# Kernel tuning notes

Hardware: AMD Instinct MI355X
Metric: run time of the kernel (lower is better)

## Reference

```python
import jax, jax.numpy as jnp
import numpy as np

B, K, H = 8, 64, 2048
NH, NKV, HD = 16, 4, 128
CTX = 4096
EPS = 1e-6


def _rope_tables(batch, total_len, head_dim):
    inv_freq = 1.0 / (10000.0 ** (np.arange(0, head_dim, 2, dtype=np.float32) / head_dim))
    pos = np.arange(total_len, dtype=np.float32)
    freqs = np.outer(pos, inv_freq)                      # [S, D/2]
    emb = np.concatenate([freqs, freqs], axis=-1)        # [S, D]
    cos = np.broadcast_to(np.cos(emb), (batch, total_len, head_dim))
    sin = np.broadcast_to(np.sin(emb), (batch, total_len, head_dim))
    return jnp.asarray(cos), jnp.asarray(sin)


def setup_inputs() -> dict:
    key = jax.random.key(0)
    ks = jax.random.split(key, 10)
    s = 0.02
    cos, sin = _rope_tables(B, CTX + K, HD)
    return {
        "hidden_states": jax.random.normal(ks[0], (B, K, H), jnp.float32),
        "ctx_k": jax.random.normal(ks[1], (B, CTX, NKV, HD), jnp.float32),
        "ctx_v": jax.random.normal(ks[2], (B, CTX, NKV, HD), jnp.float32),
        "attn_mask": jnp.zeros((B, 1, K, CTX + K), jnp.float32),
        "cos": cos,
        "sin": sin,
        "wq": jax.random.normal(ks[3], (NH * HD, H), jnp.float32) * s,
        "wk": jax.random.normal(ks[4], (NKV * HD, H), jnp.float32) * s,
        "wv": jax.random.normal(ks[5], (NKV * HD, H), jnp.float32) * s,
        "wo": jax.random.normal(ks[6], (H, NH * HD), jnp.float32) * s,
        "q_norm_w": jnp.ones((HD,), jnp.float32),
        "k_norm_w": jnp.ones((HD,), jnp.float32),
    }


def _rms_norm(x, w):
    var = jnp.mean(jnp.square(x), axis=-1, keepdims=True)
    return x * jax.lax.rsqrt(var + EPS) * w


def _rotate_half(x):
    x1, x2 = jnp.split(x, 2, axis=-1)
    return jnp.concatenate([-x2, x1], axis=-1)


def reference(hidden_states, ctx_k, ctx_v, attn_mask, cos, sin,
              wq, wk, wv, wo, q_norm_w, k_norm_w):
    b, k_len, _ = hidden_states.shape
    ctx_len = ctx_k.shape[1]
    groups = NH // NKV

    # projections -> [B, heads, S, D]
    q = (hidden_states @ wq.T).reshape(b, k_len, NH, HD).transpose(0, 2, 1, 3)
    k_noise = (hidden_states @ wk.T).reshape(b, k_len, NKV, HD).transpose(0, 2, 1, 3)
    v_noise = (hidden_states @ wv.T).reshape(b, k_len, NKV, HD).transpose(0, 2, 1, 3)

    # concat context KV (already per-head projected) with noise KV
    k = jnp.concatenate([ctx_k.transpose(0, 2, 1, 3), k_noise], axis=2)  # [B,NKV,ctx+K,D]
    v = jnp.concatenate([ctx_v.transpose(0, 2, 1, 3), v_noise], axis=2)

    # QK RMSNorm over head_dim
    q = _rms_norm(q, q_norm_w)
    k = _rms_norm(k, k_norm_w)

    # RoPE: q occupies the last K positions, k spans all ctx+K positions
    cos_q = cos[:, ctx_len:, :][:, None, :, :]
    sin_q = sin[:, ctx_len:, :][:, None, :, :]
    cos_k = cos[:, None, :, :]
    sin_k = sin[:, None, :, :]
    q = q * cos_q + _rotate_half(q) * sin_q
    k = k * cos_k + _rotate_half(k) * sin_k

    # GQA expand kv heads -> NH heads
    k = jnp.repeat(k, groups, axis=1)  # [B,NH,ctx+K,D]
    v = jnp.repeat(v, groups, axis=1)

    # scaled dot product attention with float mask
    scale = 1.0 / jnp.sqrt(jnp.float32(HD))
    scores = jnp.einsum("bhqd,bhkd->bhqk", q, k) * scale + attn_mask
    probs = jax.nn.softmax(scores, axis=-1)
    attn = jnp.einsum("bhqk,bhkd->bhqd", probs, v)

    out = attn.transpose(0, 2, 1, 3).reshape(b, k_len, NH * HD)
    return out @ wo.T
```

## Files before the change

### kernel.cpp

```cpp
#include <hip/hip_runtime.h>

#define BB   8
#define KQ   64
#define HDIM 2048
#define NH   16
#define NKV  4
#define HD   128
#define CTX  4096
#define TTOT 4160
#define NTILES 65
#define LOG2E 1.4426950408889634f
#define SCALE 0.08838834764831845f
#define QSCALE (SCALE * LOG2E)
#define MFIX 16.34f

typedef unsigned short u16;
typedef unsigned int   u32;
typedef __attribute__((ext_vector_type(8))) short  s16x8;
typedef __attribute__((ext_vector_type(4))) unsigned short u16x4;
typedef __attribute__((ext_vector_type(4))) float  f32x4;
typedef __bf16 bf16x8 __attribute__((ext_vector_type(8)));

__device__ __forceinline__ u16 f2bf(float f) {
    union { __bf16 h; u16 u; } v; v.h = (__bf16)f; return v.u;
}
__device__ __forceinline__ float bf2f(u16 u) {
    union { float f; u32 u; } v; v.u = ((u32)u) << 16;
    return v.f;
}
__device__ __forceinline__ u32 pack2(float a, float b) {
    return (u32)f2bf(a) | ((u32)f2bf(b) << 16);
}
__device__ __forceinline__ f32x4 mfma16(bf16x8 a, bf16x8 b, f32x4 c) {
    return __builtin_amdgcn_mfma_f32_16x16x32_bf16(a, b, c, 0, 0, 0);
}

__global__ __launch_bounds__(256) void cast_all(
    const float* __restrict__ wq, const float* __restrict__ wk,
    const float* __restrict__ wv, const float* __restrict__ wo,
    const float* __restrict__ hs, const float* __restrict__ cosT,
    const float* __restrict__ sinT,
    u16* __restrict__ wqkvb, u16* __restrict__ wob, u16* __restrict__ hsb,
    u16* __restrict__ cosb, u16* __restrict__ sinb)
{
    const int i = blockIdx.x * 256 + threadIdx.x;
    const float* src; u16* dst;
    if (i < 524288)        { src = wq + (size_t)i * 8;             dst = wqkvb + (size_t)i * 8; }
    else if (i < 655360)   { src = wk + (size_t)(i - 524288) * 8;  dst = wqkvb + (size_t)i * 8; }
    else if (i < 786432)   { src = wv + (size_t)(i - 655360) * 8;  dst = wqkvb + (size_t)i * 8; }
    else if (i < 1310720)  { src = wo + (size_t)(i - 786432) * 8;  dst = wob + (size_t)(i - 786432) * 8; }
    else if (i < 1441792)  { src = hs + (size_t)(i - 1310720) * 8; dst = hsb + (size_t)(i - 1310720) * 8; }
    else if (i < 1475072)  { const int l = (i - 1441792) * 8;
                             src = cosT + (size_t)(l >> 6) * 128 + (l & 63); dst = cosb + l; }
    else                   { const int l = (i - 1475072) * 8;
                             src = sinT + (size_t)(l >> 6) * 128 + (l & 63); dst = sinb + l; }
    float4 a = *(const float4*)src;
    float4 b = *(const float4*)(src + 4);
    s16x8 v;
    v[0]=(short)f2bf(a.x); v[1]=(short)f2bf(a.y); v[2]=(short)f2bf(a.z); v[3]=(short)f2bf(a.w);
    v[4]=(short)f2bf(b.x); v[5]=(short)f2bf(b.y); v[6]=(short)f2bf(b.z); v[7]=(short)f2bf(b.w);
    *(s16x8*)dst = v;
}

__global__ __launch_bounds__(256) void prep_mask(
    const float* __restrict__ mask, u16* __restrict__ maskT)
{
    __shared__ float T[64 * 65];
    const int pt = blockIdx.x % 65, b = blockIdx.x / 65;
    const int p0 = pt * 64;
    {
        const int q = threadIdx.x >> 2, pg = (threadIdx.x & 3) * 16;
        const float* src = mask + ((size_t)b * 64 + q) * TTOT + p0 + pg;
#pragma unroll
        for (int v4 = 0; v4 < 4; ++v4) {
            float4 v = *(const float4*)(src + v4 * 4);
            T[q * 65 + pg + v4 * 4 + 0] = fmaf(v.x, LOG2E, -MFIX);
            T[q * 65 + pg + v4 * 4 + 1] = fmaf(v.y, LOG2E, -MFIX);
            T[q * 65 + pg + v4 * 4 + 2] = fmaf(v.z, LOG2E, -MFIX);
            T[q * 65 + pg + v4 * 4 + 3] = fmaf(v.w, LOG2E, -MFIX);
        }
    }
    __syncthreads();
    {
        const int pos = threadIdx.x >> 2, qg = (threadIdx.x & 3) * 16;
        u16* dst = maskT + ((size_t)b * TTOT + p0 + pos) * 64 + qg;
#pragma unroll
        for (int h8 = 0; h8 < 2; ++h8) {
            s16x8 v;
#pragma unroll
            for (int je = 0; je < 8; ++je)
                v[je] = (short)f2bf(T[(qg + h8 * 8 + je) * 65 + pos]);
            *(s16x8*)(dst + h8 * 8) = v;
        }
    }
}

__device__ __forceinline__ void gemm64_body(
    const u16* __restrict__ Ab, const u16* __restrict__ Bb,
    float* __restrict__ Cb, const int ldc, const int ldk, const int Klen,
    u16* Ash, u16* Bsh)
{
    const int tid = threadIdx.x, lane = tid & 63;
    const int w = tid >> 6, wm = w >> 1, wn = w & 1;
    const int l15 = lane & 15, l4 = lane >> 4;
    const int srow = tid >> 2, scol = (tid & 3) * 16;

    f32x4 acc[2][2];
#pragma unroll
    for (int i = 0; i < 2; ++i)
#pragma unroll
        for (int j = 0; j < 2; ++j) acc[i][j] = (f32x4){0.f, 0.f, 0.f, 0.f};

    const u16* ap = Ab + (size_t)srow * ldk + scol;
    const u16* bp = Bb + (size_t)srow * ldk + scol;
    s16x8 ra0 = *(const s16x8*)ap, ra1 = *(const s16x8*)(ap + 8);
    s16x8 rb0 = *(const s16x8*)bp, rb1 = *(const s16x8*)(bp + 8);
    __builtin_amdgcn_sched_barrier(0);

    for (int k0 = 0; k0 < Klen; k0 += 64) {
        __syncthreads();
        *(s16x8*)(Ash + srow * 72 + scol)     = ra0;
        *(s16x8*)(Ash + srow * 72 + scol + 8) = ra1;
        *(s16x8*)(Bsh + srow * 72 + scol)     = rb0;
        *(s16x8*)(Bsh + srow * 72 + scol + 8) = rb1;
        __syncthreads();
        if (k0 + 64 < Klen) {
            const u16* ap2 = ap + k0 + 64;
            const u16* bp2 = bp + k0 + 64;
            ra0 = *(const s16x8*)ap2; ra1 = *(const s16x8*)(ap2 + 8);
            rb0 = *(const s16x8*)bp2; rb1 = *(const s16x8*)(bp2 + 8);
            __builtin_amdgcn_sched_barrier(0);
        }
#pragma unroll
        for (int ks = 0; ks < 2; ++ks) {
            bf16x8 am[2], bb[2];
#pragma unroll
            for (int i = 0; i < 2; ++i) {
                am[i] = *(const bf16x8*)(Ash + (wm * 32 + i * 16 + l15) * 72 + ks * 32 + l4 * 8);
                bb[i] = *(const bf16x8*)(Bsh + (wn * 32 + i * 16 + l15) * 72 + ks * 32 + l4 * 8);
            }
#pragma unroll
            for (int i = 0; i < 2; ++i)
#pragma unroll
                for (int j = 0; j < 2; ++j)
                    acc[i][j] = mfma16(am[i], bb[j], acc[i][j]);
        }
    }

    float* Cw = Cb + (size_t)(wm * 32) * ldc + wn * 32;
#pragma unroll
    for (int i = 0; i < 2; ++i)
#pragma unroll
        for (int j = 0; j < 2; ++j)
#pragma unroll
            for (int r = 0; r < 4; ++r)
                Cw[(size_t)(i * 16 + l4 * 4 + r) * ldc + j * 16 + l15] = acc[i][j][r];
}

__global__ __launch_bounds__(256) void gemm_qkv_sk(
    const u16* __restrict__ hsb, const u16* __restrict__ wqkvb,
    float* __restrict__ qkvp)
{
    __shared__ __align__(16) u16 Ash[64 * 72];
    __shared__ __align__(16) u16 Bsh[64 * 72];
    const int wid = (blockIdx.x & 7) * 192 + (blockIdx.x >> 3);
    const int y = wid >> 5, rem = wid & 31, kc = rem >> 3, x = rem & 7;
    const int koff = kc * 512;
    const u16* Ab = hsb + (size_t)x * 64 * HDIM + koff;
    const u16* Bb = wqkvb + (size_t)y * 64 * HDIM + koff;
    float* Cb = qkvp + (size_t)kc * 512 * 3072 + (size_t)x * 64 * 3072 + y * 64;
    gemm64_body(Ab, Bb, Cb, 3072, HDIM, 512, Ash, Bsh);
}

__global__ __launch_bounds__(256) void gemm_out_sk(
    const u16* __restrict__ attnb, const u16* __restrict__ wob,
    float* __restrict__ outp)
{
    __shared__ __align__(16) u16 Ash[64 * 72];
    __shared__ __align__(16) u16 Bsh[64 * 72];
    const int wid = (blockIdx.x & 7) * 128 + (blockIdx.x >> 3);
    const int y = wid >> 5, rem = wid & 31, kc = rem >> 3, x = rem & 7;
    const int koff = kc * 512;
    const u16* Ab = attnb + (size_t)x * 64 * HDIM + koff;
    const u16* Bb = wob + (size_t)y * 64 * HDIM + koff;
    float* Cb = outp + (size_t)kc * 512 * 2048 + (size_t)x * 64 * 2048 + y * 64;
    gemm64_body(Ab, Bb, Cb, 2048, HDIM, 512, Ash, Bsh);
}

__global__ __launch_bounds__(256) void reduce4(
    const float* __restrict__ p, float* __restrict__ out, const size_t chunk)
{
    const size_t i = ((size_t)blockIdx.x * 256 + threadIdx.x) * 4;
    float4 a = *(const float4*)(p + i);
    float4 b = *(const float4*)(p + i + chunk);
    float4 c = *(const float4*)(p + i + 2 * chunk);
    float4 d = *(const float4*)(p + i + 3 * chunk);
    float4 r;
    r.x = (a.x + b.x) + (c.x + d.x);
    r.y = (a.y + b.y) + (c.y + d.y);
    r.z = (a.z + b.z) + (c.z + d.z);
    r.w = (a.w + b.w) + (c.w + d.w);
    *(float4*)(out + i) = r;
}

__device__ __forceinline__ void norm_rope_vals(
    float2 xa, float2 xb, const float* __restrict__ wgt,
    const float* __restrict__ cosT, const float* __restrict__ sinT,
    int pos, int j, float outScale, u16* __restrict__ dst)
{
    float ss = xa.x * xa.x + xa.y * xa.y + xb.x * xb.x + xb.y * xb.y;
#pragma unroll
    for (int m = 1; m < 32; m <<= 1) ss += __shfl_xor(ss, m);
    const float rr = rsqrtf(ss * (1.0f / 128.0f) + 1e-6f);
    float2 wa = *(const float2*)(wgt + 2 * j);
    float2 wb = *(const float2*)(wgt + 2 * j + 64);
    float2 ca = *(const float2*)(cosT + (size_t)pos * 128 + 2 * j);
    float2 sa = *(const float2*)(sinT + (size_t)pos * 128 + 2 * j);
    const float nax = xa.x * rr * wa.x, nay = xa.y * rr * wa.y;
    const float nbx = xb.x * rr * wb.x, nby = xb.y * rr * wb.y;
    const float lox = (nax * ca.x - nbx * sa.x) * outScale;
    const float loy = (nay * ca.y - nby * sa.y) * outScale;
    const float hix = (nbx * ca.x + nax * sa.x) * outScale;
    const float hiy = (nby * ca.y + nay * sa.y) * outScale;
    ((u32*)dst)[j]      = pack2(lox, loy);
    ((u32*)dst)[j + 32] = pack2(hix, hiy);
}

__global__ __launch_bounds__(256) void finalize_qkv(
    const float* __restrict__ qkvp, const float* __restrict__ qw,
    const float* __restrict__ kw, const float* __restrict__ cosT,
    const float* __restrict__ sinT,
    u16* __restrict__ Qb, u16* __restrict__ knb, u16* __restrict__ vnb)
{
    const int unit = blockIdx.x * 8 + (threadIdx.x >> 5);
    const int j = threadIdx.x & 31;
    const int slot = unit % 24, bq = unit / 24;
    const int b = bq >> 6, q = bq & 63;
    const int col0 = (slot < 16) ? slot * 128
                   : (slot < 20) ? 2048 + (slot - 16) * 128
                                 : 2560 + (slot - 20) * 128;
    const float* base = qkvp + (size_t)bq * 3072 + col0;

    float2 xa = {0.f, 0.f}, xb = {0.f, 0.f};
#pragma unroll
    for (int kc = 0; kc < 4; ++kc) {
        const float* p = base + (size_t)kc * 512 * 3072;
        float2 a = *(const float2*)(p + 2 * j);
        float2 c = *(const float2*)(p + 2 * j + 64);
        xa.x += a.x; xa.y += a.y; xb.x += c.x; xb.y += c.y;
    }

    if (slot < 16) {
        norm_rope_vals(xa, xb, qw, cosT, sinT, CTX + q, j, QSCALE,
                       Qb + ((size_t)((b * 16 + slot) * 64 + q)) * 128);
    } else if (slot < 20) {
        norm_rope_vals(xa, xb, kw, cosT, sinT, CTX + q, j, 1.0f,
                       knb + ((size_t)((b * 4 + (slot - 16)) * 64 + q)) * 128);
    } else {
        u16* dst = vnb + ((size_t)((b * 4 + (slot - 20)) * 64 + q)) * 128;
        ((u32*)dst)[j]      = pack2(xa.x, xa.y);
        ((u32*)dst)[j + 32] = pack2(xb.x, xb.y);
    }
}

__global__ __launch_bounds__(256) void build_ctx_v(
    const float* __restrict__ ctxv, const u16* __restrict__ vnb,
    u16* __restrict__ VtG)
{
    __shared__ __align__(16) float Vt[64 * 130];
    const int bid = blockIdx.x;
    if (bid < 2048) {
        const int pt = bid & 63, kv = (bid >> 6) & 3, b = bid >> 8;
        const int p0 = pt * 64;
        const float* src = ctxv + ((size_t)(b * 4096 + p0) * 4 + kv) * 128;
#pragma unroll
        for (int it = 0; it < 8; ++it) {
            const int g = it * 256 + threadIdx.x;
            const int row = g >> 5, c4 = (g & 31) * 4;
            *(float4*)(&Vt[row * 130 + c4]) = *(const float4*)(src + (size_t)row * 512 + c4);
        }
        __syncthreads();
        const int d = threadIdx.x & 127, half = threadIdx.x >> 7;
        u16* dst = VtG + ((size_t)(b * 4 + kv) * 128 + d) * TTOT + p0 + half * 32;
#pragma unroll
        for (int q8 = 0; q8 < 4; ++q8) {
            s16x8 v;
#pragma unroll
            for (int je = 0; je < 8; ++je)
                v[je] = (short)f2bf(Vt[(half * 32 + q8 * 8 + je) * 130 + d]);
            *(s16x8*)(dst + q8 * 8) = v;
        }
    } else {
        const int idx = bid - 2048;
        const u16* src = vnb + (size_t)idx * 64 * 128;
        u16* dstb = VtG + (size_t)idx * 128 * TTOT + 4096;
        const int d = threadIdx.x & 127, qh = threadIdx.x >> 7;
        u16* dst = dstb + (size_t)d * TTOT + qh * 32;
#pragma unroll
        for (int q8 = 0; q8 < 4; ++q8) {
            s16x8 v;
#pragma unroll
            for (int je = 0; je < 8; ++je)
                v[je] = (short)src[(size_t)(qh * 32 + q8 * 8 + je) * 128 + d];
            *(s16x8*)(dst + q8 * 8) = v;
        }
    }
}

template <int S>
__global__ __launch_bounds__(512, 2) void attn_partial(
    const u16* __restrict__ Qb, const float* __restrict__ ctxk,
    const float* __restrict__ knw, const u16* __restrict__ cosb,
    const u16* __restrict__ sinb, const u16* __restrict__ knb,
    const u16* __restrict__ VtG, const u16* __restrict__ maskT,
    u16* __restrict__ Opart, float* __restrict__ lsum)
{
    __shared__ __align__(16) u16 Ksh[2][64 * 136];
    __shared__ __align__(16) u16 Vsh[2][128 * 72];
    __shared__ __align__(16) u16 Msh[2][64 * 72];
    __shared__ __align__(16) u16 Psh[8][32 * 40];

    const int s = blockIdx.x, kv = blockIdx.y, b = blockIdx.z;
    const int tid = threadIdx.x, lane = tid & 63, w = tid >> 6;
    const int h = kv * 4 + (w >> 1);
    const int qh = w & 1, qbase = qh * 32;
    const int l15 = lane & 15, l4 = lane >> 4;
    const int t0 = (NTILES * s) / S, t1 = (NTILES * (s + 1)) / S;

    const int krow = tid >> 3, kg8 = (tid & 7) * 8;
    const int vr = tid >> 3, vc8 = (tid & 7) * 8;
    const int mpos = tid >> 3, mq8 = (tid & 7) * 8;

    const float4 w0 = *(const float4*)(knw + kg8);
    const float4 w1 = *(const float4*)(knw + kg8 + 4);
    const float4 w2 = *(const float4*)(knw + kg8 + 64);
    const float4 w3 = *(const float4*)(knw + kg8 + 68);

    bf16x8 aq[2][4];
    {
        const u16* qb = Qb + ((size_t)((b * 16 + h) * 64 + qbase)) * 128;
#pragma unroll
        for (int mt = 0; mt < 2; ++mt)
#pragma unroll
            for (int ks = 0; ks < 4; ++ks)
                aq[mt][ks] = *(const bf16x8*)(qb + (mt * 16 + l15) * 128 + ks * 32 + l4 * 8);
    }

    bf16x8 bones;
    {
        __bf16 e = (l15 == 0) ? (__bf16)1.0f : (__bf16)0.0f;
#pragma unroll
        for (int i = 0; i < 8; ++i) bones[i] = e;
    }

    f32x4 o[2][8], ol[2];
#pragma unroll
    for (int mt = 0; mt < 2; ++mt) {
        ol[mt] = (f32x4){0.f, 0.f, 0.f, 0.f};
#pragma unroll
        for (int nt = 0; nt < 8; ++nt) o[mt][nt] = (f32x4){0.f, 0.f, 0.f, 0.f};
    }

    const u16* Kn    = knb + (size_t)(b * 4 + kv) * 64 * 128;
    const u16* Vbase = VtG + (size_t)(b * 4 + kv) * 128 * TTOT;
    const u16* mrow  = maskT + (size_t)b * TTOT * 64;
    u16* P = Psh[w];

    float4 rx0, rx1, rx2, rx3;
    s16x8 rcs, rsn;
    s16x8 rkn0, rkn1;
    s16x8 rv0, rv1, rm;
    int tin = -1;

    auto ld = [&](int t) {
        const int p = t * 64;
        if (t < 64) {
            const float* kp_ = ctxk + (((size_t)(b * 4096 + p + krow)) * 4 + kv) * 128 + kg8;
            rx0 = *(const float4*)kp_;        rx1 = *(const float4*)(kp_ + 4);
            rx2 = *(const float4*)(kp_ + 64); rx3 = *(const float4*)(kp_ + 68);
            rcs = *(const s16x8*)(cosb + (size_t)(p + krow) * 64 + kg8);
            rsn = *(const s16x8*)(sinb + (size_t)(p + krow) * 64 + kg8);
        } else {
            const u16* kp2 = Kn + (size_t)krow * 128 + kg8;
            rkn0 = *(const s16x8*)kp2;
            rkn1 = *(const s16x8*)(kp2 + 64);
        }
        rv0 = *(const s16x8*)(Vbase + (size_t)vr * TTOT + p + vc8);
        rv1 = *(const s16x8*)(Vbase + (size_t)(vr + 64) * TTOT + p + vc8);
        rm  = *(const s16x8*)(mrow + (size_t)(p + mpos) * 64 + mq8);
        tin = t;
        __builtin_amdgcn_sched_barrier(0);
    };
    auto st = [&](int buf) {
        if (tin < 64) {
            float ss = rx0.x*rx0.x + rx0.y*rx0.y + rx0.z*rx0.z + rx0.w*rx0.w
                     + rx1.x*rx1.x + rx1.y*rx1.y + rx1.z*rx1.z + rx1.w*rx1.w
                     + rx2.x*rx2.x + rx2.y*rx2.y + rx2.z*rx2.z + rx2.w*rx2.w
                     + rx3.x*rx3.x + rx3.y*rx3.y + rx3.z*rx3.z + rx3.w*rx3.w;
            ss += __shfl_xor(ss, 1);
            ss += __shfl_xor(ss, 2);
            ss += __shfl_xor(ss, 4);
            const float rr = rsqrtf(ss * (1.0f / 128.0f) + 1e-6f);
            s16x8 klo, khi;
#define KROPE(i, xl, xh, wl, wh)                                     \
            {                                                        \
                const float nlo = xl * rr * wl, nhi = xh * rr * wh;  \
                const float c = bf2f((u16)rcs[i]), sn = bf2f((u16)rsn[i]); \
                klo[i] = (short)f2bf(nlo * c - nhi * sn);            \
                khi[i] = (short)f2bf(nhi * c + nlo * sn);            \
            }
            KROPE(0, rx0.x, rx2.x, w0.x, w2.x)
            KROPE(1, rx0.y, rx2.y, w0.y, w2.y)
            KROPE(2, rx0.z, rx2.z, w0.z, w2.z)
            KROPE(3, rx0.w, rx2.w, w0.w, w2.w)
            KROPE(4, rx1.x, rx3.x, w1.x, w3.x)
            KROPE(5, rx1.y, rx3.y, w1.y, w3.y)
            KROPE(6, rx1.z, rx3.z, w1.z, w3.z)
            KROPE(7, rx1.w, rx3.w, w1.w, w3.w)
#undef KROPE
            *(s16x8*)(Ksh[buf] + krow * 136 + kg8)      = klo;
            *(s16x8*)(Ksh[buf] + krow * 136 + 64 + kg8) = khi;
        } else {
            *(s16x8*)(Ksh[buf] + krow * 136 + kg8)      = rkn0;
            *(s16x8*)(Ksh[buf] + krow * 136 + 64 + kg8) = rkn1;
        }
        *(s16x8*)(Vsh[buf] + vr * 72 + vc8) = rv0;
        *(s16x8*)(Vsh[buf] + (vr + 64) * 72 + vc8) = rv1;
        *(s16x8*)(Msh[buf] + mpos * 72 + mq8) = rm;
    };

    ld(t0);
    st(0);
    __syncthreads();
    if (t0 + 1 < t1) ld(t0 + 1);

    int cur = 0;
    for (int t = t0; t < t1; ++t) {
        f32x4 sc[2][4];
#pragma unroll
        for (int mt = 0; mt < 2; ++mt)
#pragma unroll
            for (int nt = 0; nt < 4; ++nt) sc[mt][nt] = (f32x4){0.f, 0.f, 0.f, 0.f};
        __builtin_amdgcn_s_setprio(1);
#pragma unroll
        for (int nt = 0; nt < 4; ++nt) {
#pragma unroll
            for (int ks = 0; ks < 4; ++ks) {
                bf16x8 bk = *(const bf16x8*)(Ksh[cur] + (nt * 16 + l15) * 136 + ks * 32 + l4 * 8);
                sc[0][nt] = mfma16(aq[0][ks], bk, sc[0][nt]);
                sc[1][nt] = mfma16(aq[1][ks], bk, sc[1][nt]);
            }
        }
        __builtin_amdgcn_s_setprio(0);

#pragma unroll
        for (int mt = 0; mt < 2; ++mt) {
#pragma unroll
            for (int nt = 0; nt < 4; ++nt) {
                u16x4 m4 = *(const u16x4*)(Msh[cur] + (nt * 16 + l15) * 72 + qbase + mt * 16 + l4 * 4);
#pragma unroll
                for (int r = 0; r < 4; ++r)
                    sc[mt][nt][r] = exp2f(sc[mt][nt][r] + bf2f(m4[r]));
            }
        }

#pragma unroll
        for (int ks = 0; ks < 2; ++ks) {
#pragma unroll
            for (int mt = 0; mt < 2; ++mt)
#pragma unroll
                for (int r = 0; r < 4; ++r) {
                    P[(mt * 16 + l4 * 4 + r) * 40 + l15]      = f2bf(sc[mt][ks * 2 + 0][r]);
                    P[(mt * 16 + l4 * 4 + r) * 40 + 16 + l15] = f2bf(sc[mt][ks * 2 + 1][r]);
                }
            bf16x8 ap0 = *(const bf16x8*)(P + (l15) * 40 + l4 * 8);
            bf16x8 ap1 = *(const bf16x8*)(P + (16 + l15) * 40 + l4 * 8);
            __builtin_amdgcn_s_setprio(1);
#pragma unroll
            for (int nt = 0; nt < 8; ++nt) {
                bf16x8 bv = *(const bf16x8*)(Vsh[cur] + (nt * 16 + l15) * 72 + ks * 32 + l4 * 8);
                o[0][nt] = mfma16(ap0, bv, o[0][nt]);
                o[1][nt] = mfma16(ap1, bv, o[1][nt]);
            }
            ol[0] = mfma16(ap0, bones, ol[0]);
            ol[1] = mfma16(ap1, bones, ol[1]);
            __builtin_amdgcn_s_setprio(0);
        }

        if (t + 1 < t1) st(cur ^ 1);
        __syncthreads();
        if (t + 2 < t1) ld(t + 2);
        cur ^= 1;
    }

    {
        u16* ob = Opart + ((size_t)((b * 16 + h) * S + s)) * 8192;
#pragma unroll
        for (int mt = 0; mt < 2; ++mt)
#pragma unroll
            for (int nt = 0; nt < 8; ++nt) {
                u16x4 v;
#pragma unroll
                for (int r = 0; r < 4; ++r) v[r] = f2bf(o[mt][nt][r]);
                *(u16x4*)(ob + (((qh * 2 + mt) * 8 + nt) * 64 + lane) * 4) = v;
            }
        if (l15 == 0) {
#pragma unroll
            for (int mt = 0; mt < 2; ++mt)
#pragma unroll
                for (int r = 0; r < 4; ++r) {
                    const int q = qbase + mt * 16 + l4 * 4 + r;
                    lsum[((size_t)((b * 16 + h) * 64 + q)) * S + s] = ol[mt][r];
                }
        }
    }
}

template <int S>
__global__ __launch_bounds__(256) void merge_kernel(
    const u16* __restrict__ Opart, const float* __restrict__ lsum, u16* __restrict__ attnb)
{
    const int wid = blockIdx.x * 4 + (threadIdx.x >> 6);
    const int lane = threadIdx.x & 63;
    const int l15 = lane & 15, l4 = lane >> 4;
    const int qh = wid & 1, bh = wid >> 1;
    const int h = bh & 15, b = bh >> 4;

    float L = 0.f;
    {
        const float* lr = lsum + ((size_t)bh * 64 + qh * 32 + (lane & 31)) * S;
#pragma unroll
        for (int s2 = 0; s2 < S; ++s2) L += lr[s2];
    }
    const float invL = 1.0f / L;

    float acc[2][8][4];
#pragma unroll
    for (int mt = 0; mt < 2; ++mt)
#pragma unroll
        for (int nt = 0; nt < 8; ++nt)
#pragma unroll
            for (int r = 0; r < 4; ++r) acc[mt][nt][r] = 0.f;

    for (int s2 = 0; s2 < S; ++s2) {
        const u16* ob = Opart + ((size_t)(bh * S + s2)) * 8192;
#pragma unroll
        for (int mt = 0; mt < 2; ++mt)
#pragma unroll
            for (int nt = 0; nt < 8; ++nt) {
                u16x4 v = *(const u16x4*)(ob + (((qh * 2 + mt) * 8 + nt) * 64 + lane) * 4);
#pragma unroll
                for (int r = 0; r < 4; ++r) acc[mt][nt][r] += bf2f(v[r]);
            }
    }

#pragma unroll
    for (int mt = 0; mt < 2; ++mt)
#pragma unroll
        for (int r = 0; r < 4; ++r) {
            const float wl = __shfl(invL, mt * 16 + l4 * 4 + r);
            const int q = qh * 32 + mt * 16 + l4 * 4 + r;
            u16* dst = attnb + (size_t)(b * 64 + q) * 2048 + h * 128;
#pragma unroll
            for (int nt = 0; nt < 8; ++nt)
                dst[nt * 16 + l15] = f2bf(acc[mt][nt][r] * wl);
        }
}

extern "C" void kernel_launch(void* const* d_in, const int* in_sizes, int n_in,
                              void* d_out, int out_size, void* d_ws, size_t ws_size,
                              hipStream_t stream)
{
    (void)in_sizes; (void)n_in; (void)out_size; (void)ws_size;
    const float* hs   = (const float*)d_in[0];
    const float* ctxk = (const float*)d_in[1];
    const float* ctxv = (const float*)d_in[2];
    const float* mask = (const float*)d_in[3];
    const float* cosT = (const float*)d_in[4];
    const float* sinT = (const float*)d_in[5];
    const float* wq   = (const float*)d_in[6];
    const float* wk   = (const float*)d_in[7];
    const float* wv   = (const float*)d_in[8];
    const float* wo   = (const float*)d_in[9];
    const float* qnw  = (const float*)d_in[10];
    const float* knw  = (const float*)d_in[11];

    const int S = 8;

    char* ws = (char*)d_ws;
    size_t off = 0;
    auto carve = [&](size_t bytes) -> void* {
        void* p = ws + off;
        off += (bytes + 255) & ~(size_t)255;
        return p;
    };
    u16*   Qb    = (u16*)carve((size_t)BB * NH * 64 * 128 * 2);
    u16*   VtG   = (u16*)carve((size_t)BB * NKV * TTOT * 128 * 2);
    u16*   Opart = (u16*)carve((size_t)BB * NH * S * 8192 * 2);
    float* lsumb = (float*)carve((size_t)BB * NH * 64 * S * 4);
    u16*   attnb = (u16*)carve((size_t)512 * 2048 * 2);
    u16*   wob   = (u16*)carve((size_t)2048 * 2048 * 2);
    u16*   wqkvb = (u16*)carve((size_t)3072 * 2048 * 2);
    u16*   knb   = (u16*)carve((size_t)BB * NKV * 64 * 128 * 2);
    u16*   vnb   = (u16*)carve((size_t)BB * NKV * 64 * 128 * 2);
    u16*   maskT = (u16*)carve((size_t)BB * TTOT * 64 * 2);
    u16*   cosb  = (u16*)carve((size_t)TTOT * 64 * 2);
    u16*   sinb  = (u16*)carve((size_t)TTOT * 64 * 2);
    float* qkvp = (float*)VtG;
    u16*   hsb  = (u16*)Opart;
    float* outp = (float*)Opart;

    cast_all<<<5892, 256, 0, stream>>>(wq, wk, wv, wo, hs, cosT, sinT,
                                       wqkvb, wob, hsb, cosb, sinb);
    prep_mask<<<520, 256, 0, stream>>>(mask, maskT);
    gemm_qkv_sk<<<1536, 256, 0, stream>>>(hsb, wqkvb, qkvp);
    finalize_qkv<<<1536, 256, 0, stream>>>(qkvp, qnw, knw, cosT, sinT, Qb, knb, vnb);
    build_ctx_v<<<2080, 256, 0, stream>>>(ctxv, vnb, VtG);
    attn_partial<8><<<dim3(8, NKV, BB), 512, 0, stream>>>(
        Qb, ctxk, knw, cosb, sinb, knb, VtG, maskT, Opart, lsumb);
    merge_kernel<8><<<64, 256, 0, stream>>>(Opart, lsumb, attnb);
    gemm_out_sk<<<1024, 256, 0, stream>>>(attnb, wob, outp);
    reduce4<<<1024, 256, 0, stream>>>(outp, (float*)d_out, (size_t)512 * 2048);
}
```

Measured before the change: 133.1 us.

## Double attention block to 1024 threads with 16-row query tiles per wave

Attention partial kernel now launches 1024 threads per block: 16 waves each handle a 16-query slice instead of 8 waves handling 32 queries. Loading work is split so the first 512 threads stage K (with RMSNorm+RoPE) and the other 512 stage V and mask, which halves per-thread load/convert work. This is meant to raise latency hiding and cut per-wave register use, but it halves K/V reuse per wave (each K fragment now feeds one MFMA instead of two) and drops the 2-blocks-per-CU occupancy hint.

```diff
diff --git a/kernel.cpp b/kernel.cpp
--- a/kernel.cpp
+++ b/kernel.cpp
@@ -308,7 +308,7 @@
 }
 
 template <int S>
-__global__ __launch_bounds__(512, 2) void attn_partial(
+__global__ __launch_bounds__(1024) void attn_partial(
     const u16* __restrict__ Qb, const float* __restrict__ ctxk,
     const float* __restrict__ knw, const u16* __restrict__ cosb,
     const u16* __restrict__ sinb, const u16* __restrict__ knb,
@@ -318,32 +318,32 @@
     __shared__ __align__(16) u16 Ksh[2][64 * 136];
     __shared__ __align__(16) u16 Vsh[2][128 * 72];
     __shared__ __align__(16) u16 Msh[2][64 * 72];
-    __shared__ __align__(16) u16 Psh[8][32 * 40];
+    __shared__ __align__(16) u16 Psh[16][16 * 40];
 
     const int s = blockIdx.x, kv = blockIdx.y, b = blockIdx.z;
     const int tid = threadIdx.x, lane = tid & 63, w = tid >> 6;
-    const int h = kv * 4 + (w >> 1);
-    const int qh = w & 1, qbase = qh * 32;
+    const int h = kv * 4 + (w >> 2);
+    const int qq = w & 3, qbase = qq * 16;
     const int l15 = lane & 15, l4 = lane >> 4;
     const int t0 = (NTILES * s) / S, t1 = (NTILES * (s + 1)) / S;
-
-    const int krow = tid >> 3, kg8 = (tid & 7) * 8;
-    const int vr = tid >> 3, vc8 = (tid & 7) * 8;
-    const int mpos = tid >> 3, mq8 = (tid & 7) * 8;
+    const bool isK = (tid < 512);
+    const int tid2 = tid & 511;
+
+    const int krow = tid2 >> 3, kg8 = (tid2 & 7) * 8;
+    const int vr = tid2 >> 2, vc = (tid2 & 3) * 16;
+    const int mpos = tid2 >> 3, mq8 = (tid2 & 7) * 8;
 
     const float4 w0 = *(const float4*)(knw + kg8);
     const float4 w1 = *(const float4*)(knw + kg8 + 4);
     const float4 w2 = *(const float4*)(knw + kg8 + 64);
     const float4 w3 = *(const float4*)(knw + kg8 + 68);
 
-    bf16x8 aq[2][4];
+    bf16x8 aq[4];
     {
         const u16* qb = Qb + ((size_t)((b * 16 + h) * 64 + qbase)) * 128;
 #pragma unroll
-        for (int mt = 0; mt < 2; ++mt)
-#pragma unroll
-            for (int ks = 0; ks < 4; ++ks)
-                aq[mt][ks] = *(const bf16x8*)(qb + (mt * 16 + l15) * 128 + ks * 32 + l4 * 8);
+        for (int ks = 0; ks < 4; ++ks)
+            aq[ks] = *(const bf16x8*)(qb + l15 * 128 + ks * 32 + l4 * 8);
     }
 
     bf16x8 bones;
@@ -353,13 +353,10 @@
         for (int i = 0; i < 8; ++i) bones[i] = e;
     }
 
-    f32x4 o[2][8], ol[2];
-#pragma unroll
-    for (int mt = 0; mt < 2; ++mt) {
-        ol[mt] = (f32x4){0.f, 0.f, 0.f, 0.f};
-#pragma unroll
-        for (int nt = 0; nt < 8; ++nt) o[mt][nt] = (f32x4){0.f, 0.f, 0.f, 0.f};
-    }
+    f32x4 o[8], ol;
+    ol = (f32x4){0.f, 0.f, 0.f, 0.f};
+#pragma unroll
+    for (int nt = 0; nt < 8; ++nt) o[nt] = (f32x4){0.f, 0.f, 0.f, 0.f};
 
     const u16* Kn    = knb + (size_t)(b * 4 + kv) * 64 * 128;
     const u16* Vbase = VtG + (size_t)(b * 4 + kv) * 128 * TTOT;
@@ -374,59 +371,65 @@
 
     auto ld = [&](int t) {
         const int p = t * 64;
-        if (t < 64) {
-            const float* kp_ = ctxk + (((size_t)(b * 4096 + p + krow)) * 4 + kv) * 128 + kg8;
-            rx0 = *(const float4*)kp_;        rx1 = *(const float4*)(kp_ + 4);
-            rx2 = *(const float4*)(kp_ + 64); rx3 = *(const float4*)(kp_ + 68);
-            rcs = *(const s16x8*)(cosb + (size_t)(p + krow) * 64 + kg8);
-            rsn = *(const s16x8*)(sinb + (size_t)(p + krow) * 64 + kg8);
+        if (isK) {
+            if (t < 64) {
+                const float* kp_ = ctxk + (((size_t)(b * 4096 + p + krow)) * 4 + kv) * 128 + kg8;
+                rx0 = *(const float4*)kp_;        rx1 = *(const float4*)(kp_ + 4);
+                rx2 = *(const float4*)(kp_ + 64); rx3 = *(const float4*)(kp_ + 68);
+                rcs = *(const s16x8*)(cosb + (size_t)(p + krow) * 64 + kg8);
+                rsn = *(const s16x8*)(sinb + (size_t)(p + krow) * 64 + kg8);
+            } else {
+                const u16* kp2 = Kn + (size_t)krow * 128 + kg8;
+                rkn0 = *(const s16x8*)kp2;
+                rkn1 = *(const s16x8*)(kp2 + 64);
+            }
         } else {
-            const u16* kp2 = Kn + (size_t)krow * 128 + kg8;
-            rkn0 = *(const s16x8*)kp2;
-            rkn1 = *(const s16x8*)(kp2 + 64);
-        }
-        rv0 = *(const s16x8*)(Vbase + (size_t)vr * TTOT + p + vc8);
-        rv1 = *(const s16x8*)(Vbase + (size_t)(vr + 64) * TTOT + p + vc8);
-        rm  = *(const s16x8*)(mrow + (size_t)(p + mpos) * 64 + mq8);
+            rv0 = *(const s16x8*)(Vbase + (size_t)vr * TTOT + p + vc);
+            rv1 = *(const s16x8*)(Vbase + (size_t)vr * TTOT + p + vc + 8);
+            rm  = *(const s16x8*)(mrow + (size_t)(p + mpos) * 64 + mq8);
+        }
         tin = t;
         __builtin_amdgcn_sched_barrier(0);
     };
     auto st = [&](int buf) {
-        if (tin < 64) {
-            float ss = rx0.x*rx0.x + rx0.y*rx0.y + rx0.z*rx0.z + rx0.w*rx0.w
-                     + rx1.x*rx1.x + rx1.y*rx1.y + rx1.z*rx1.z + rx1.w*rx1.w
-                     + rx2.x*rx2.x + rx2.y*rx2.y + rx2.z*rx2.z + rx2.w*rx2.w
-                     + rx3.x*rx3.x + rx3.y*rx3.y + rx3.z*rx3.z + rx3.w*rx3.w;
-            ss += __shfl_xor(ss, 1);
-            ss += __shfl_xor(ss, 2);
-            ss += __shfl_xor(ss, 4);
-            const float rr = rsqrtf(ss * (1.0f / 128.0f) + 1e-6f);
-            s16x8 klo, khi;
+        if (isK) {
+            if (tin < 64) {
+                float ss = rx0.x*rx0.x + rx0.y*rx0.y + rx0.z*rx0.z + rx0.w*rx0.w
+                         + rx1.x*rx1.x + rx1.y*rx1.y + rx1.z*rx1.z + rx1.w*rx1.w
+                         + rx2.x*rx2.x + rx2.y*rx2.y + rx2.z*rx2.z + rx2.w*rx2.w
+                         + rx3.x*rx3.x + rx3.y*rx3.y + rx3.z*rx3.z + rx3.w*rx3.w;
+                ss += __shfl_xor(ss, 1);
+                ss += __shfl_xor(ss, 2);
+                ss += __shfl_xor(ss, 4);
+                const float rr = rsqrtf(ss * (1.0f / 128.0f) + 1e-6f);
+                s16x8 klo, khi;
 #define KROPE(i, xl, xh, wl, wh)                                     \
-            {                                                        \
-                const float nlo = xl * rr * wl, nhi = xh * rr * wh;  \
-                const float c = bf2f((u16)rcs[i]), sn = bf2f((u16)rsn[i]); \
-                klo[i] = (short)f2bf(nlo * c - nhi * sn);            \
-                khi[i] = (short)f2bf(nhi * c + nlo * sn);            \
-            }
-            KROPE(0, rx0.x, rx2.x, w0.x, w2.x)
-            KROPE(1, rx0.y, rx2.y, w0.y, w2.y)
-            KROPE(2, rx0.z, rx2.z, w0.z, w2.z)
-            KROPE(3, rx0.w, rx2.w, w0.w, w2.w)
-            KROPE(4, rx1.x, rx3.x, w1.x, w3.x)
-            KROPE(5, rx1.y, rx3.y, w1.y, w3.y)
-            KROPE(6, rx1.z, rx3.z, w1.z, w3.z)
-            KROPE(7, rx1.w, rx3.w, w1.w, w3.w)
+                {                                                    \
+                    const float nlo = xl * rr * wl, nhi = xh * rr * wh; \
+                    const float c = bf2f((u16)rcs[i]), sn = bf2f((u16)rsn[i]); \
+                    klo[i] = (short)f2bf(nlo * c - nhi * sn);        \
+                    khi[i] = (short)f2bf(nhi * c + nlo * sn);        \
+                }
+                KROPE(0, rx0.x, rx2.x, w0.x, w2.x)
+                KROPE(1, rx0.y, rx2.y, w0.y, w2.y)
+                KROPE(2, rx0.z, rx2.z, w0.z, w2.z)
+                KROPE(3, rx0.w, rx2.w, w0.w, w2.w)
+                KROPE(4, rx1.x, rx3.x, w1.x, w3.x)
+                KROPE(5, rx1.y, rx3.y, w1.y, w3.y)
+                KROPE(6, rx1.z, rx3.z, w1.z, w3.z)
+                KROPE(7, rx1.w, rx3.w, w1.w, w3.w)
 #undef KROPE
-            *(s16x8*)(Ksh[buf] + krow * 136 + kg8)      = klo;
-            *(s16x8*)(Ksh[buf] + krow * 136 + 64 + kg8) = khi;
+                *(s16x8*)(Ksh[buf] + krow * 136 + kg8)      = klo;
+                *(s16x8*)(Ksh[buf] + krow * 136 + 64 + kg8) = khi;
+            } else {
+                *(s16x8*)(Ksh[buf] + krow * 136 + kg8)      = rkn0;
+                *(s16x8*)(Ksh[buf] + krow * 136 + 64 + kg8) = rkn1;
+            }
         } else {
-            *(s16x8*)(Ksh[buf] + krow * 136 + kg8)      = rkn0;
-            *(s16x8*)(Ksh[buf] + krow * 136 + 64 + kg8) = rkn1;
-        }
-        *(s16x8*)(Vsh[buf] + vr * 72 + vc8) = rv0;
-        *(s16x8*)(Vsh[buf] + (vr + 64) * 72 + vc8) = rv1;
-        *(s16x8*)(Msh[buf] + mpos * 72 + mq8) = rm;
+            *(s16x8*)(Vsh[buf] + vr * 72 + vc)     = rv0;
+            *(s16x8*)(Vsh[buf] + vr * 72 + vc + 8) = rv1;
+            *(s16x8*)(Msh[buf] + mpos * 72 + mq8)  = rm;
+        }
     };
 
     ld(t0);
@@ -436,54 +439,43 @@
 
     int cur = 0;
     for (int t = t0; t < t1; ++t) {
-        f32x4 sc[2][4];
-#pragma unroll
-        for (int mt = 0; mt < 2; ++mt)
-#pragma unroll
-            for (int nt = 0; nt < 4; ++nt) sc[mt][nt] = (f32x4){0.f, 0.f, 0.f, 0.f};
+        f32x4 sc[4];
+#pragma unroll
+        for (int nt = 0; nt < 4; ++nt) sc[nt] = (f32x4){0.f, 0.f, 0.f, 0.f};
         __builtin_amdgcn_s_setprio(1);
 #pragma unroll
         for (int nt = 0; nt < 4; ++nt) {
 #pragma unroll
             for (int ks = 0; ks < 4; ++ks) {
                 bf16x8 bk = *(const bf16x8*)(Ksh[cur] + (nt * 16 + l15) * 136 + ks * 32 + l4 * 8);
-                sc[0][nt] = mfma16(aq[0][ks], bk, sc[0][nt]);
-                sc[1][nt] = mfma16(aq[1][ks], bk, sc[1][nt]);
+                sc[nt] = mfma16(aq[ks], bk, sc[nt]);
             }
         }
         __builtin_amdgcn_s_setprio(0);
 
 #pragma unroll
-        for (int mt = 0; mt < 2; ++mt) {
-#pragma unroll
-            for (int nt = 0; nt < 4; ++nt) {
-                u16x4 m4 = *(const u16x4*)(Msh[cur] + (nt * 16 + l15) * 72 + qbase + mt * 16 + l4 * 4);
-#pragma unroll
-                for (int r = 0; r < 4; ++r)
-                    sc[mt][nt][r] = exp2f(sc[mt][nt][r] + bf2f(m4[r]));
-            }
+        for (int nt = 0; nt < 4; ++nt) {
+            u16x4 m4 = *(const u16x4*)(Msh[cur] + (nt * 16 + l15) * 72 + qbase + l4 * 4);
+#pragma unroll
+            for (int r = 0; r < 4; ++r)
+                sc[nt][r] = exp2f(sc[nt][r] + bf2f(m4[r]));
         }
 
 #pragma unroll
         for (int ks = 0; ks < 2; ++ks) {
 #pragma unroll
-            for (int mt = 0; mt < 2; ++mt)
-#pragma unroll
-                for (int r = 0; r < 4; ++r) {
-                    P[(mt * 16 + l4 * 4 + r) * 40 + l15]      = f2bf(sc[mt][ks * 2 + 0][r]);
-                    P[(mt * 16 + l4 * 4 + r) * 40 + 16 + l15] = f2bf(sc[mt][ks * 2 + 1][r]);
-                }
-            bf16x8 ap0 = *(const bf16x8*)(P + (l15) * 40 + l4 * 8);
-            bf16x8 ap1 = *(const bf16x8*)(P + (16 + l15) * 40 + l4 * 8);
+            for (int r = 0; r < 4; ++r) {
+                P[(l4 * 4 + r) * 40 + l15]      = f2bf(sc[ks * 2 + 0][r]);
+                P[(l4 * 4 + r) * 40 + 16 + l15] = f2bf(sc[ks * 2 + 1][r]);
+            }
+            bf16x8 ap = *(const bf16x8*)(P + l15 * 40 + l4 * 8);
             __builtin_amdgcn_s_setprio(1);
 #pragma unroll
             for (int nt = 0; nt < 8; ++nt) {
                 bf16x8 bv = *(const bf16x8*)(Vsh[cur] + (nt * 16 + l15) * 72 + ks * 32 + l4 * 8);
-                o[0][nt] = mfma16(ap0, bv, o[0][nt]);
-                o[1][nt] = mfma16(ap1, bv, o[1][nt]);
-            }
-            ol[0] = mfma16(ap0, bones, ol[0]);
-            ol[1] = mfma16(ap1, bones, ol[1]);
+                o[nt] = mfma16(ap, bv, o[nt]);
+            }
+            ol = mfma16(ap, bones, ol);
             __builtin_amdgcn_s_setprio(0);
         }
 
@@ -494,24 +486,20 @@
     }
 
     {
-        u16* ob = Opart + ((size_t)((b * 16 + h) * S + s)) * 8192;
-#pragma unroll
-        for (int mt = 0; mt < 2; ++mt)
-#pragma unroll
-            for (int nt = 0; nt < 8; ++nt) {
-                u16x4 v;
-#pragma unroll
-                for (int r = 0; r < 4; ++r) v[r] = f2bf(o[mt][nt][r]);
-                *(u16x4*)(ob + (((qh * 2 + mt) * 8 + nt) * 64 + lane) * 4) = v;
-            }
+        u16* ob = Opart + ((size_t)((b * 16 + h) * S + s)) * 8192 + qq * 2048;
+#pragma unroll
+        for (int nt = 0; nt < 8; ++nt) {
+            u16x4 v;
+#pragma unroll
+            for (int r = 0; r < 4; ++r) v[r] = f2bf(o[nt][r]);
+            *(u16x4*)(ob + nt * 256 + lane * 4) = v;
+        }
         if (l15 == 0) {
 #pragma unroll
-            for (int mt = 0; mt < 2; ++mt)
-#pragma unroll
-                for (int r = 0; r < 4; ++r) {
-                    const int q = qbase + mt * 16 + l4 * 4 + r;
-                    lsum[((size_t)((b * 16 + h) * 64 + q)) * S + s] = ol[mt][r];
-                }
+            for (int r = 0; r < 4; ++r) {
+                const int q = qbase + l4 * 4 + r;
+                lsum[((size_t)((b * 16 + h) * 64 + q)) * S + s] = ol[r];
+            }
         }
     }
 }
@@ -616,7 +604,7 @@
     gemm_qkv_sk<<<1536, 256, 0, stream>>>(hsb, wqkvb, qkvp);
     finalize_qkv<<<1536, 256, 0, stream>>>(qkvp, qnw, knw, cosT, sinT, Qb, knb, vnb);
     build_ctx_v<<<2080, 256, 0, stream>>>(ctxv, vnb, VtG);
-    attn_partial<8><<<dim3(8, NKV, BB), 512, 0, stream>>>(
+    attn_partial<8><<<dim3(8, NKV, BB), 1024, 0, stream>>>(
         Qb, ctxk, knw, cosb, sinb, knb, VtG, maskT, Opart, lsumb);
     merge_kernel<8><<<64, 256, 0, stream>>>(Opart, lsumb, attnb);
     gemm_out_sk<<<1024, 256, 0, stream>>>(attnb, wob, outp);
```

New measurement: 186.8 us. 1.4x slower.
